# Kernel tuning notes

Measured on AMD Instinct MI355X. Metric: run time of the kernel, lower is better.

The kernel has to match this reference:

```python
import jax, jax.numpy as jnp
import numpy as np

N_NODES = 100000
N_EDGES = 1600000
IN_FEATS = 128
H_FEATS = 128
NUM_CLASSES = 1


def setup_inputs() -> dict:
    key = jax.random.key(0)
    ks = jax.random.split(key, 12)
    node_feat = jax.random.normal(ks[0], (N_NODES, IN_FEATS), dtype=jnp.float32)
    edge_feat = jax.random.normal(ks[1], (N_EDGES, 1), dtype=jnp.float32)
    src = jax.random.randint(ks[2], (N_EDGES,), 0, N_NODES)
    dst = jax.random.randint(ks[3], (N_EDGES,), 0, N_NODES)
    d_in1 = 2 * IN_FEATS + 1
    d_mid = 2 * H_FEATS + 1
    s1 = 1.0 / np.sqrt(d_in1)
    sm = 1.0 / np.sqrt(d_mid)
    W1 = jax.random.uniform(ks[4], (d_in1, H_FEATS), jnp.float32, -s1, s1)
    b1 = jax.random.uniform(ks[5], (H_FEATS,), jnp.float32, -s1, s1)
    Wmid = jax.random.uniform(ks[6], (8, d_mid, H_FEATS), jnp.float32, -sm, sm)
    bmid = jax.random.uniform(ks[7], (8, H_FEATS), jnp.float32, -sm, sm)
    W2 = jax.random.uniform(ks[8], (d_mid, NUM_CLASSES), jnp.float32, -sm, sm)
    b2 = jax.random.uniform(ks[9], (NUM_CLASSES,), jnp.float32, -sm, sm)
    return {"node_feat": node_feat, "edge_feat": edge_feat, "src": src, "dst": dst,
            "W1": W1, "b1": b1, "Wmid": Wmid, "bmid": bmid, "W2": W2, "b2": b2}


def _sage_conv(hn, he, src, dst, W, b):
    # copy_u + sum: aggregate source node features at destination nodes
    hn_aggr = jax.ops.segment_sum(hn[src], dst, num_segments=N_NODES)
    # copy_e + sum: aggregate edge features at destination nodes -> [N, 1]
    he_aggr = jax.ops.segment_sum(he, dst, num_segments=N_NODES)
    h_total = jnp.concatenate([hn, hn_aggr, he_aggr], axis=1)
    return h_total @ W + b


def reference(node_feat, edge_feat, src, dst, W1, b1, Wmid, bmid, W2, b2):
    h = _sage_conv(node_feat, edge_feat, src, dst, W1, b1)
    h = jax.nn.relu(h) + h
    # mid layers 1-4: relu residual
    for i in range(4):
        h = _sage_conv(h, edge_feat, src, dst, Wmid[i], bmid[i])
        h = jax.nn.relu(h) + h
    # mid layer 5: sigmoid (no residual)
    h = _sage_conv(h, edge_feat, src, dst, Wmid[4], bmid[4])
    h = jax.nn.sigmoid(h)
    # mid layers 6-7: relu residual
    for i in range(5, 7):
        h = _sage_conv(h, edge_feat, src, dst, Wmid[i], bmid[i])
        h = jax.nn.relu(h) + h
    # mid layer 8: sigmoid (no residual)
    h = _sage_conv(h, edge_feat, src, dst, Wmid[7], bmid[7])
    h = jax.nn.sigmoid(h)
    # output layer
    h = _sage_conv(h, edge_feat, src, dst, W2, b2)
    return h
```

## Files before the change

kernel.cpp:

```cpp
#include <hip/hip_runtime.h>

#define N_NODES 100000
#define N_EDGES 1600000
#define HF 128
#define BCAP 64

typedef unsigned int uint;
typedef __attribute__((ext_vector_type(8))) short short8;
typedef __attribute__((ext_vector_type(4))) float f32x4;

__device__ __forceinline__ unsigned short f2bf(float f) {
    uint u = __float_as_uint(f);
    uint r = (u + 0x7fff + ((u >> 16) & 1)) >> 16;
    return (unsigned short)r;
}
__device__ __forceinline__ float bf2f_u(uint bits16) {
    return __uint_as_float(bits16 << 16);
}


__global__ void fill_bucket_kernel(const int* __restrict__ src, const int* __restrict__ dst,
                                   const float* __restrict__ ef, int* __restrict__ cur,
                                   int* __restrict__ cs, float* __restrict__ efb, int base) {
    const int Q = N_EDGES / 8;
    int i = blockIdx.x * blockDim.x + threadIdx.x;
    if (i >= Q) return;
    int d[4], s[4]; float f[4];
    #pragma unroll
    for (int k = 0; k < 4; ++k) {
        int e = base + i + k * Q;
        d[k] = dst[e]; s[k] = src[e]; f[k] = ef[e];
    }
    int p[4];
    #pragma unroll
    for (int k = 0; k < 4; ++k) p[k] = atomicAdd(&cur[d[k]], 1);
    #pragma unroll
    for (int k = 0; k < 4; ++k)
        if (p[k] < BCAP) {
            cs[(size_t)d[k] * BCAP + p[k]]  = s[k];
            efb[(size_t)d[k] * BCAP + p[k]] = f[k];
        }
}

__global__ void he_kernel(const float* __restrict__ efb, const int* __restrict__ cnt,
                          float* __restrict__ he) {
    int t = threadIdx.x;
    int node = blockIdx.x * 16 + (t >> 4);
    int gl = t & 15;
    if (node >= N_NODES) return;
    int cn = cnt[node]; if (cn > BCAP) cn = BCAP;
    const float* bk = efb + (size_t)node * BCAP;
    float s = 0.f;
    for (int e = gl; e < cn; e += 16) s += bk[e];
    s += __shfl_xor(s, 1); s += __shfl_xor(s, 2);
    s += __shfl_xor(s, 4); s += __shfl_xor(s, 8);
    if (gl == 0) he[node] = s;
}


__global__ void conv_h_kernel(const float* __restrict__ in, unsigned short* __restrict__ out) {
    int i = (blockIdx.x * 256 + threadIdx.x) * 4;
    float4 v = *(const float4*)(in + i);
    uint2 o;
    o.x = (uint)f2bf(v.x) | ((uint)f2bf(v.y) << 16);
    o.y = (uint)f2bf(v.z) | ((uint)f2bf(v.w) << 16);
    *(uint2*)(out + i) = o;
}

__global__ void conv_w_kernel(const float* __restrict__ W1, const float* __restrict__ Wmid,
                              unsigned short* __restrict__ Wt) {
    int id = blockIdx.x * 256 + threadIdx.x;
    if (id >= 9 * 32768) return;
    int layer = id >> 15;
    int rem = id & 32767;
    int kc = rem >> 10;
    int c  = (rem >> 3) & 127;
    int e  = rem & 7;
    const float* Wl = (layer == 0) ? W1 : Wmid + (size_t)(layer - 1) * 257 * 128;
    Wt[(size_t)layer * 32768 + rem] = f2bf(Wl[(size_t)(kc * 8 + e) * 128 + c]);
}

__global__ void conv_wcb_kernel(const float* __restrict__ W1, const float* __restrict__ b1,
                                const float* __restrict__ Wmid, const float* __restrict__ bmid,
                                float* __restrict__ wcarr, float* __restrict__ barr) {
    int id = blockIdx.x * 256 + threadIdx.x;
    if (id >= 9 * 128) return;
    int layer = id >> 7, c = id & 127;
    const float* Wl = (layer == 0) ? W1 : Wmid + (size_t)(layer - 1) * 257 * 128;
    const float* bl = (layer == 0) ? b1 : bmid + (size_t)(layer - 1) * 128;
    wcarr[id] = Wl[256 * 128 + c];
    barr[id]  = bl[c];
}


__device__ __forceinline__ void accum8(float* lo, float* hi, uint4 v) {
    lo[0] += __uint_as_float(v.x << 16); hi[0] += __uint_as_float(v.x & 0xffff0000u);
    lo[1] += __uint_as_float(v.y << 16); hi[1] += __uint_as_float(v.y & 0xffff0000u);
    lo[2] += __uint_as_float(v.z << 16); hi[2] += __uint_as_float(v.z & 0xffff0000u);
    lo[3] += __uint_as_float(v.w << 16); hi[3] += __uint_as_float(v.w & 0xffff0000u);
}

__launch_bounds__(256, 6)
__global__ void fused_layer_kernel(const unsigned short* __restrict__ X,
                                   unsigned short* __restrict__ Y,
                                   const int* __restrict__ cnt,
                                   const int* __restrict__ cs,
                                   const float* __restrict__ he,
                                   const unsigned short* __restrict__ Wt,
                                   const float* __restrict__ wcarr,
                                   const float* __restrict__ barr,
                                   int mode) {
    __shared__ short gtile[64 * 128];
    int t = threadIdx.x;
    int row0 = blockIdx.x * 64;
    int gl = t & 15;
    const uint4* hu = (const uint4*)X;
    const uint NM1 = N_NODES - 1;

    for (int pass = 0; pass < 4; ++pass) {
        int r = pass * 16 + (t >> 4);
        int node = row0 + r;
        float alo[4] = {0.f,0.f,0.f,0.f}, ahi[4] = {0.f,0.f,0.f,0.f};
        float blo[4] = {0.f,0.f,0.f,0.f}, bhi[4] = {0.f,0.f,0.f,0.f};
        if (node < N_NODES) {
            int cn = cnt[node]; if (cn > BCAP) cn = BCAP;
            const int4* bk4 = (const int4*)(cs + (size_t)node * BCAP);
            int4 q0 = bk4[0], q1 = bk4[1];
            for (int e = 0; e < cn; e += 8) {
                int4 c0 = q0, c1 = q1;
                if (e + 8 < cn) {
                    int b = (e + 8) >> 2;
                    q0 = bk4[b]; q1 = bk4[b + 1];
                }
                uint i0 = min((uint)c0.x, NM1), i1 = min((uint)c0.y, NM1);
                uint i2 = min((uint)c0.z, NM1), i3 = min((uint)c0.w, NM1);
                uint i4 = min((uint)c1.x, NM1), i5 = min((uint)c1.y, NM1);
                uint i6 = min((uint)c1.z, NM1), i7 = min((uint)c1.w, NM1);
                uint4 v0 = hu[(size_t)i0 * 16 + gl];
                uint4 v1 = hu[(size_t)i1 * 16 + gl];
                uint4 v2 = hu[(size_t)i2 * 16 + gl];
                uint4 v3 = hu[(size_t)i3 * 16 + gl];
                uint4 v4 = hu[(size_t)i4 * 16 + gl];
                uint4 v5 = hu[(size_t)i5 * 16 + gl];
                uint4 v6 = hu[(size_t)i6 * 16 + gl];
                uint4 v7 = hu[(size_t)i7 * 16 + gl];
                accum8(alo, ahi, v0);
                if (e + 1 < cn) accum8(blo, bhi, v1);
                if (e + 2 < cn) accum8(alo, ahi, v2);
                if (e + 3 < cn) accum8(blo, bhi, v3);
                if (e + 4 < cn) accum8(alo, ahi, v4);
                if (e + 5 < cn) accum8(blo, bhi, v5);
                if (e + 6 < cn) accum8(alo, ahi, v6);
                if (e + 7 < cn) accum8(blo, bhi, v7);
            }
        }
        uint4 o;
        o.x = (uint)f2bf(alo[0] + blo[0]) | ((uint)f2bf(ahi[0] + bhi[0]) << 16);
        o.y = (uint)f2bf(alo[1] + blo[1]) | ((uint)f2bf(ahi[1] + bhi[1]) << 16);
        o.z = (uint)f2bf(alo[2] + blo[2]) | ((uint)f2bf(ahi[2] + bhi[2]) << 16);
        o.w = (uint)f2bf(alo[3] + blo[3]) | ((uint)f2bf(ahi[3] + bhi[3]) << 16);
        int off = r * 256 + gl * 16;
        off ^= (r & 7) << 4;
        *(uint4*)((char*)gtile + off) = o;
    }
    __syncthreads();

    int w = t >> 6, lane = t & 63;
    int l15 = lane & 15, l4 = lane >> 4;
    int rloc = (w >> 1) * 32;
    int rb = row0 + rloc;
    int cb = (w & 1) * 64;

    f32x4 acc[2][4] = {};

    #pragma unroll
    for (int ks = 0; ks < 8; ++ks) {
        int kk = (ks & 3) * 32 + l4 * 8;
        short8 a[2];
        if (ks < 4) {
            #pragma unroll
            for (int ra = 0; ra < 2; ++ra) {
                int row = rb + ra * 16 + l15;
                if (row > N_NODES - 1) row = N_NODES - 1;
                a[ra] = *(const short8*)((const short*)X + (size_t)row * 128 + kk);
            }
        } else {
            #pragma unroll
            for (int ra = 0; ra < 2; ++ra) {
                int r = rloc + ra * 16 + l15;
                int off = r * 256 + kk * 2;
                off ^= (r & 7) << 4;
                a[ra] = *(const short8*)((const char*)gtile + off);
            }
        }
        short8 b[4];
        const short* wt = (const short*)Wt + (size_t)(ks * 4 + l4) * 1024;
        #pragma unroll
        for (int cf = 0; cf < 4; ++cf) {
            int c = cb + cf * 16 + l15;
            b[cf] = *(const short8*)(wt + c * 8);
        }
        #pragma unroll
        for (int cf = 0; cf < 4; ++cf)
            #pragma unroll
            for (int ra = 0; ra < 2; ++ra)
                acc[ra][cf] = __builtin_amdgcn_mfma_f32_16x16x32_bf16(a[ra], b[cf], acc[ra][cf], 0, 0, 0);
    }

    float wcv[4], bbv[4];
    #pragma unroll
    for (int cf = 0; cf < 4; ++cf) {
        int c = cb + cf * 16 + l15;
        wcv[cf] = wcarr[c];
        bbv[cf] = barr[c];
    }
    #pragma unroll
    for (int ra = 0; ra < 2; ++ra) {
        #pragma unroll
        for (int j = 0; j < 4; ++j) {
            int row = rb + ra * 16 + l4 * 4 + j;
            if (row >= N_NODES) continue;
            float hv = he[row];
            #pragma unroll
            for (int cf = 0; cf < 4; ++cf) {
                int c = cb + cf * 16 + l15;
                float z = acc[ra][cf][j] + hv * wcv[cf] + bbv[cf];
                if (mode == 0) z += fmaxf(z, 0.f);
                else           z = 1.f / (1.f + __expf(-z));
                Y[(size_t)row * 128 + c] = f2bf(z);
            }
        }
    }
}


__global__ void dot_kernel(const unsigned short* __restrict__ h, const float* __restrict__ W2,
                           float* __restrict__ p) {
    int t = threadIdx.x;
    int node = blockIdx.x * 16 + (t >> 4);
    int gl = t & 15;
    if (node >= N_NODES) return;
    uint4 v = ((const uint4*)h)[(size_t)node * 16 + gl];
    const float* wseg = W2 + 128 + gl * 8;
    float s = bf2f_u(v.x & 0xffffu) * wseg[0] + bf2f_u(v.x >> 16) * wseg[1]
            + bf2f_u(v.y & 0xffffu) * wseg[2] + bf2f_u(v.y >> 16) * wseg[3]
            + bf2f_u(v.z & 0xffffu) * wseg[4] + bf2f_u(v.z >> 16) * wseg[5]
            + bf2f_u(v.w & 0xffffu) * wseg[6] + bf2f_u(v.w >> 16) * wseg[7];
    s += __shfl_xor(s, 1); s += __shfl_xor(s, 2);
    s += __shfl_xor(s, 4); s += __shfl_xor(s, 8);
    if (gl == 0) p[node] = s;
}

__global__ void final2_kernel(const unsigned short* __restrict__ h, const float* __restrict__ p,
                              const int* __restrict__ cnt, const int* __restrict__ cs,
                              const float* __restrict__ he, const float* __restrict__ W2,
                              const float* __restrict__ b2, float* __restrict__ out) {
    int t = threadIdx.x;
    int node = blockIdx.x * 16 + (t >> 4);
    int gl = t & 15;
    if (node >= N_NODES) return;
    uint4 v = ((const uint4*)h)[(size_t)node * 16 + gl];
    const float* wseg = W2 + gl * 8;
    float s = bf2f_u(v.x & 0xffffu) * wseg[0] + bf2f_u(v.x >> 16) * wseg[1]
            + bf2f_u(v.y & 0xffffu) * wseg[2] + bf2f_u(v.y >> 16) * wseg[3]
            + bf2f_u(v.z & 0xffffu) * wseg[4] + bf2f_u(v.z >> 16) * wseg[5]
            + bf2f_u(v.w & 0xffffu) * wseg[6] + bf2f_u(v.w >> 16) * wseg[7];
    int cn = cnt[node]; if (cn > BCAP) cn = BCAP;
    const int* bk = cs + (size_t)node * BCAP;
    for (int e = gl; e < cn; e += 16) s += p[bk[e]];
    s += __shfl_xor(s, 1); s += __shfl_xor(s, 2);
    s += __shfl_xor(s, 4); s += __shfl_xor(s, 8);
    if (gl == 0) out[node] = s + he[node] * W2[256] + b2[0];
}


extern "C" void kernel_launch(void* const* d_in, const int* in_sizes, int n_in,
                              void* d_out, int out_size, void* d_ws, size_t ws_size,
                              hipStream_t stream) {
    const float* node_feat = (const float*)d_in[0];
    const float* edge_feat = (const float*)d_in[1];
    const int*   src  = (const int*)d_in[2];
    const int*   dst  = (const int*)d_in[3];
    const float* W1   = (const float*)d_in[4];
    const float* b1   = (const float*)d_in[5];
    const float* Wmid = (const float*)d_in[6];
    const float* bmid = (const float*)d_in[7];
    const float* W2   = (const float*)d_in[8];
    const float* b2   = (const float*)d_in[9];
    float* out = (float*)d_out;

    char* ws = (char*)d_ws;
    size_t off = 0;
    auto carve = [&](size_t bytes) {
        void* p = ws + off;
        off = (off + bytes + 255) & ~(size_t)255;
        return p;
    };
    int*   cur  = (int*)carve((size_t)N_NODES * 4);
    float* he   = (float*)carve((size_t)N_NODES * 4);
    int*   cs   = (int*)carve((size_t)N_NODES * BCAP * 4);
    float* efb  = (float*)carve((size_t)N_NODES * BCAP * 4);
    unsigned short* h0 = (unsigned short*)carve((size_t)N_NODES * HF * 2);
    unsigned short* h1 = (unsigned short*)carve((size_t)N_NODES * HF * 2);
    unsigned short* Wt = (unsigned short*)carve((size_t)9 * 32768 * 2);
    float* wcarr = (float*)carve((size_t)9 * 128 * 4);
    float* barr  = (float*)carve((size_t)9 * 128 * 4);
    float* pbuf  = (float*)carve((size_t)N_NODES * 4);
    (void)ws_size; (void)in_sizes; (void)n_in; (void)out_size;

    hipMemsetAsync(cur, 0, (size_t)N_NODES * 4, stream);
    const int fillGrid = (N_EDGES / 8 + 255) / 256;
    fill_bucket_kernel<<<dim3(fillGrid), dim3(256), 0, stream>>>(
        src, dst, edge_feat, cur, cs, efb, 0);
    fill_bucket_kernel<<<dim3(fillGrid), dim3(256), 0, stream>>>(
        src, dst, edge_feat, cur, cs, efb, N_EDGES / 2);
    he_kernel<<<dim3((N_NODES + 15) / 16), dim3(256), 0, stream>>>(efb, cur, he);

    conv_h_kernel<<<dim3(12500), dim3(256), 0, stream>>>(node_feat, h0);
    conv_w_kernel<<<dim3((9 * 32768 + 255) / 256), dim3(256), 0, stream>>>(W1, Wmid, Wt);
    conv_wcb_kernel<<<dim3(5), dim3(256), 0, stream>>>(W1, b1, Wmid, bmid, wcarr, barr);

    const int gemmGrid = (N_NODES + 63) / 64;
    unsigned short* hbuf[2] = { h0, h1 };

    for (int L = 0; L < 9; ++L) {
        int mode = (L == 5 || L == 8) ? 1 : 0;
        fused_layer_kernel<<<dim3(gemmGrid), dim3(256), 0, stream>>>(
            hbuf[L & 1], hbuf[(L + 1) & 1], cur, cs, he,
            Wt + (size_t)L * 32768, wcarr + L * 128, barr + L * 128, mode);
    }
    const unsigned short* hf = hbuf[1];
    dot_kernel<<<dim3((N_NODES + 15) / 16), dim3(256), 0, stream>>>(hf, W2, pbuf);
    final2_kernel<<<dim3((N_NODES + 15) / 16), dim3(256), 0, stream>>>(
        hf, pbuf, cur, cs, he, W2, b2, out);
}
```

Before: 829.8 us.

## Bucket edges by source-node group and pack source index with bf16 edge feature

Edges for each destination are split into 8 sub-buckets by source-id range, so the gather loop in each layer walks groups in order and all rows of a block touch similar regions of the feature table at the same time, aiming for better L2 locality. Each bucket entry packs the 17-bit source index with a truncated bf16 edge feature into one word, which removes the separate edge-feature bucket array. The cost is a larger bucket array and an 8x larger counter array, plus a per-group cap of 16 that can drop edges whenever a group overflows. Group boundaries are not synchronised across threads, so the intended locality relies on per-group timing lining up on its own.

```diff
diff --git a/kernel.cpp b/kernel.cpp
--- a/kernel.cpp
+++ b/kernel.cpp
@@ -3,7 +3,9 @@
 #define N_NODES 100000
 #define N_EDGES 1600000
 #define HF 128
-#define BCAP 64
+#define NGRP 8
+#define GCAP 16
+#define BKSZ (NGRP * GCAP)
 
 typedef unsigned int uint;
 typedef __attribute__((ext_vector_type(8))) short short8;
@@ -17,41 +19,48 @@
 __device__ __forceinline__ float bf2f_u(uint bits16) {
     return __uint_as_float(bits16 << 16);
 }
+__device__ __forceinline__ uint src_group(uint s) {
+    return (uint)(((unsigned long long)s * 687195ull) >> 33);
+}
 
 
 __global__ void fill_bucket_kernel(const int* __restrict__ src, const int* __restrict__ dst,
-                                   const float* __restrict__ ef, int* __restrict__ cur,
-                                   int* __restrict__ cs, float* __restrict__ efb, int base) {
+                                   const float* __restrict__ ef, int* __restrict__ gcnt,
+                                   uint* __restrict__ cs, int base) {
     const int Q = N_EDGES / 8;
     int i = blockIdx.x * blockDim.x + threadIdx.x;
     if (i >= Q) return;
-    int d[4], s[4]; float f[4];
+    int d[4]; uint ent[4], g[4];
     #pragma unroll
     for (int k = 0; k < 4; ++k) {
         int e = base + i + k * Q;
-        d[k] = dst[e]; s[k] = src[e]; f[k] = ef[e];
+        d[k] = dst[e];
+        uint s = (uint)src[e];
+        ent[k] = (s << 15) | ((uint)f2bf(ef[e]) >> 1);
+        g[k] = src_group(s);
     }
     int p[4];
     #pragma unroll
-    for (int k = 0; k < 4; ++k) p[k] = atomicAdd(&cur[d[k]], 1);
+    for (int k = 0; k < 4; ++k) p[k] = atomicAdd(&gcnt[d[k] * NGRP + g[k]], 1);
     #pragma unroll
     for (int k = 0; k < 4; ++k)
-        if (p[k] < BCAP) {
-            cs[(size_t)d[k] * BCAP + p[k]]  = s[k];
-            efb[(size_t)d[k] * BCAP + p[k]] = f[k];
-        }
-}
-
-__global__ void he_kernel(const float* __restrict__ efb, const int* __restrict__ cnt,
+        if (p[k] < GCAP)
+            cs[(size_t)d[k] * BKSZ + g[k] * GCAP + p[k]] = ent[k];
+}
+
+__global__ void he_kernel(const uint* __restrict__ cs, const int* __restrict__ gcnt,
                           float* __restrict__ he) {
     int t = threadIdx.x;
     int node = blockIdx.x * 16 + (t >> 4);
     int gl = t & 15;
     if (node >= N_NODES) return;
-    int cn = cnt[node]; if (cn > BCAP) cn = BCAP;
-    const float* bk = efb + (size_t)node * BCAP;
+    const uint* bk = cs + (size_t)node * BKSZ;
     float s = 0.f;
-    for (int e = gl; e < cn; e += 16) s += bk[e];
+    #pragma unroll
+    for (int g = 0; g < NGRP; ++g) {
+        int cn = gcnt[node * NGRP + g]; if (cn > GCAP) cn = GCAP;
+        if (gl < cn) s += __uint_as_float((bk[g * GCAP + gl] & 0x7fffu) << 17);
+    }
     s += __shfl_xor(s, 1); s += __shfl_xor(s, 2);
     s += __shfl_xor(s, 4); s += __shfl_xor(s, 8);
     if (gl == 0) he[node] = s;
@@ -93,18 +102,18 @@
 }
 
 
-__device__ __forceinline__ void accum8(float* lo, float* hi, uint4 v) {
-    lo[0] += __uint_as_float(v.x << 16); hi[0] += __uint_as_float(v.x & 0xffff0000u);
-    lo[1] += __uint_as_float(v.y << 16); hi[1] += __uint_as_float(v.y & 0xffff0000u);
-    lo[2] += __uint_as_float(v.z << 16); hi[2] += __uint_as_float(v.z & 0xffff0000u);
-    lo[3] += __uint_as_float(v.w << 16); hi[3] += __uint_as_float(v.w & 0xffff0000u);
+__device__ __forceinline__ void accum8lh(float* a, uint4 v) {
+    a[0] += __uint_as_float(v.x << 16); a[4] += __uint_as_float(v.x & 0xffff0000u);
+    a[1] += __uint_as_float(v.y << 16); a[5] += __uint_as_float(v.y & 0xffff0000u);
+    a[2] += __uint_as_float(v.z << 16); a[6] += __uint_as_float(v.z & 0xffff0000u);
+    a[3] += __uint_as_float(v.w << 16); a[7] += __uint_as_float(v.w & 0xffff0000u);
 }
 
 __launch_bounds__(256, 6)
 __global__ void fused_layer_kernel(const unsigned short* __restrict__ X,
                                    unsigned short* __restrict__ Y,
-                                   const int* __restrict__ cnt,
-                                   const int* __restrict__ cs,
+                                   const int* __restrict__ gcnt,
+                                   const uint* __restrict__ cs,
                                    const float* __restrict__ he,
                                    const unsigned short* __restrict__ Wt,
                                    const float* __restrict__ wcarr,
@@ -117,48 +126,45 @@
     const uint4* hu = (const uint4*)X;
     const uint NM1 = N_NODES - 1;
 
-    for (int pass = 0; pass < 4; ++pass) {
-        int r = pass * 16 + (t >> 4);
-        int node = row0 + r;
-        float alo[4] = {0.f,0.f,0.f,0.f}, ahi[4] = {0.f,0.f,0.f,0.f};
-        float blo[4] = {0.f,0.f,0.f,0.f}, bhi[4] = {0.f,0.f,0.f,0.f};
-        if (node < N_NODES) {
-            int cn = cnt[node]; if (cn > BCAP) cn = BCAP;
-            const int4* bk4 = (const int4*)(cs + (size_t)node * BCAP);
-            int4 q0 = bk4[0], q1 = bk4[1];
-            for (int e = 0; e < cn; e += 8) {
-                int4 c0 = q0, c1 = q1;
-                if (e + 8 < cn) {
-                    int b = (e + 8) >> 2;
-                    q0 = bk4[b]; q1 = bk4[b + 1];
-                }
-                uint i0 = min((uint)c0.x, NM1), i1 = min((uint)c0.y, NM1);
-                uint i2 = min((uint)c0.z, NM1), i3 = min((uint)c0.w, NM1);
-                uint i4 = min((uint)c1.x, NM1), i5 = min((uint)c1.y, NM1);
-                uint i6 = min((uint)c1.z, NM1), i7 = min((uint)c1.w, NM1);
+    float acc[4][8];
+    #pragma unroll
+    for (int p4 = 0; p4 < 4; ++p4)
+        #pragma unroll
+        for (int j = 0; j < 8; ++j) acc[p4][j] = 0.f;
+
+    for (int g = 0; g < NGRP; ++g) {
+        #pragma unroll
+        for (int pass = 0; pass < 4; ++pass) {
+            int node = row0 + pass * 16 + (t >> 4);
+            if (node >= N_NODES) continue;
+            int cn = gcnt[node * NGRP + g]; if (cn > GCAP) cn = GCAP;
+            if (cn == 0) continue;
+            const uint* bk = cs + (size_t)node * BKSZ + g * GCAP;
+            uint4 q = *(const uint4*)bk;
+            for (int e = 0; e < cn; e += 4) {
+                uint4 c = q;
+                if (e + 4 < cn) q = *(const uint4*)(bk + e + 4);
+                uint i0 = min(c.x >> 15, NM1), i1 = min(c.y >> 15, NM1);
+                uint i2 = min(c.z >> 15, NM1), i3 = min(c.w >> 15, NM1);
                 uint4 v0 = hu[(size_t)i0 * 16 + gl];
                 uint4 v1 = hu[(size_t)i1 * 16 + gl];
                 uint4 v2 = hu[(size_t)i2 * 16 + gl];
                 uint4 v3 = hu[(size_t)i3 * 16 + gl];
-                uint4 v4 = hu[(size_t)i4 * 16 + gl];
-                uint4 v5 = hu[(size_t)i5 * 16 + gl];
-                uint4 v6 = hu[(size_t)i6 * 16 + gl];
-                uint4 v7 = hu[(size_t)i7 * 16 + gl];
-                accum8(alo, ahi, v0);
-                if (e + 1 < cn) accum8(blo, bhi, v1);
-                if (e + 2 < cn) accum8(alo, ahi, v2);
-                if (e + 3 < cn) accum8(blo, bhi, v3);
-                if (e + 4 < cn) accum8(alo, ahi, v4);
-                if (e + 5 < cn) accum8(blo, bhi, v5);
-                if (e + 6 < cn) accum8(alo, ahi, v6);
-                if (e + 7 < cn) accum8(blo, bhi, v7);
+                accum8lh(acc[pass], v0);
+                if (e + 1 < cn) accum8lh(acc[pass], v1);
+                if (e + 2 < cn) accum8lh(acc[pass], v2);
+                if (e + 3 < cn) accum8lh(acc[pass], v3);
             }
         }
+    }
+    #pragma unroll
+    for (int pass = 0; pass < 4; ++pass) {
+        int r = pass * 16 + (t >> 4);
         uint4 o;
-        o.x = (uint)f2bf(alo[0] + blo[0]) | ((uint)f2bf(ahi[0] + bhi[0]) << 16);
-        o.y = (uint)f2bf(alo[1] + blo[1]) | ((uint)f2bf(ahi[1] + bhi[1]) << 16);
-        o.z = (uint)f2bf(alo[2] + blo[2]) | ((uint)f2bf(ahi[2] + bhi[2]) << 16);
-        o.w = (uint)f2bf(alo[3] + blo[3]) | ((uint)f2bf(ahi[3] + bhi[3]) << 16);
+        o.x = (uint)f2bf(acc[pass][0]) | ((uint)f2bf(acc[pass][4]) << 16);
+        o.y = (uint)f2bf(acc[pass][1]) | ((uint)f2bf(acc[pass][5]) << 16);
+        o.z = (uint)f2bf(acc[pass][2]) | ((uint)f2bf(acc[pass][6]) << 16);
+        o.w = (uint)f2bf(acc[pass][3]) | ((uint)f2bf(acc[pass][7]) << 16);
         int off = r * 256 + gl * 16;
         off ^= (r & 7) << 4;
         *(uint4*)((char*)gtile + off) = o;
@@ -171,7 +177,7 @@
     int rb = row0 + rloc;
     int cb = (w & 1) * 64;
 
-    f32x4 acc[2][4] = {};
+    f32x4 macc[2][4] = {};
 
     #pragma unroll
     for (int ks = 0; ks < 8; ++ks) {
@@ -204,7 +210,7 @@
         for (int cf = 0; cf < 4; ++cf)
             #pragma unroll
             for (int ra = 0; ra < 2; ++ra)
-                acc[ra][cf] = __builtin_amdgcn_mfma_f32_16x16x32_bf16(a[ra], b[cf], acc[ra][cf], 0, 0, 0);
+                macc[ra][cf] = __builtin_amdgcn_mfma_f32_16x16x32_bf16(a[ra], b[cf], macc[ra][cf], 0, 0, 0);
     }
 
     float wcv[4], bbv[4];
@@ -224,7 +230,7 @@
             #pragma unroll
             for (int cf = 0; cf < 4; ++cf) {
                 int c = cb + cf * 16 + l15;
-                float z = acc[ra][cf][j] + hv * wcv[cf] + bbv[cf];
+                float z = macc[ra][cf][j] + hv * wcv[cf] + bbv[cf];
                 if (mode == 0) z += fmaxf(z, 0.f);
                 else           z = 1.f / (1.f + __expf(-z));
                 Y[(size_t)row * 128 + c] = f2bf(z);
@@ -252,7 +258,7 @@
 }
 
 __global__ void final2_kernel(const unsigned short* __restrict__ h, const float* __restrict__ p,
-                              const int* __restrict__ cnt, const int* __restrict__ cs,
+                              const int* __restrict__ gcnt, const uint* __restrict__ cs,
                               const float* __restrict__ he, const float* __restrict__ W2,
                               const float* __restrict__ b2, float* __restrict__ out) {
     int t = threadIdx.x;
@@ -265,9 +271,13 @@
             + bf2f_u(v.y & 0xffffu) * wseg[2] + bf2f_u(v.y >> 16) * wseg[3]
             + bf2f_u(v.z & 0xffffu) * wseg[4] + bf2f_u(v.z >> 16) * wseg[5]
             + bf2f_u(v.w & 0xffffu) * wseg[6] + bf2f_u(v.w >> 16) * wseg[7];
-    int cn = cnt[node]; if (cn > BCAP) cn = BCAP;
-    const int* bk = cs + (size_t)node * BCAP;
-    for (int e = gl; e < cn; e += 16) s += p[bk[e]];
+    const uint NM1 = N_NODES - 1;
+    const uint* bk = cs + (size_t)node * BKSZ;
+    #pragma unroll
+    for (int g = 0; g < NGRP; ++g) {
+        int cn = gcnt[node * NGRP + g]; if (cn > GCAP) cn = GCAP;
+        if (gl < cn) s += p[min(bk[g * GCAP + gl] >> 15, NM1)];
+    }
     s += __shfl_xor(s, 1); s += __shfl_xor(s, 2);
     s += __shfl_xor(s, 4); s += __shfl_xor(s, 8);
     if (gl == 0) out[node] = s + he[node] * W2[256] + b2[0];
@@ -296,10 +306,9 @@
         off = (off + bytes + 255) & ~(size_t)255;
         return p;
     };
-    int*   cur  = (int*)carve((size_t)N_NODES * 4);
+    int*   gcnt = (int*)carve((size_t)N_NODES * NGRP * 4);
     float* he   = (float*)carve((size_t)N_NODES * 4);
-    int*   cs   = (int*)carve((size_t)N_NODES * BCAP * 4);
-    float* efb  = (float*)carve((size_t)N_NODES * BCAP * 4);
+    uint*  cs   = (uint*)carve((size_t)N_NODES * BKSZ * 4);
     unsigned short* h0 = (unsigned short*)carve((size_t)N_NODES * HF * 2);
     unsigned short* h1 = (unsigned short*)carve((size_t)N_NODES * HF * 2);
     unsigned short* Wt = (unsigned short*)carve((size_t)9 * 32768 * 2);
@@ -308,13 +317,13 @@
     float* pbuf  = (float*)carve((size_t)N_NODES * 4);
     (void)ws_size; (void)in_sizes; (void)n_in; (void)out_size;
 
-    hipMemsetAsync(cur, 0, (size_t)N_NODES * 4, stream);
+    hipMemsetAsync(gcnt, 0, (size_t)N_NODES * NGRP * 4, stream);
     const int fillGrid = (N_EDGES / 8 + 255) / 256;
     fill_bucket_kernel<<<dim3(fillGrid), dim3(256), 0, stream>>>(
-        src, dst, edge_feat, cur, cs, efb, 0);
+        src, dst, edge_feat, gcnt, cs, 0);
     fill_bucket_kernel<<<dim3(fillGrid), dim3(256), 0, stream>>>(
-        src, dst, edge_feat, cur, cs, efb, N_EDGES / 2);
-    he_kernel<<<dim3((N_NODES + 15) / 16), dim3(256), 0, stream>>>(efb, cur, he);
+        src, dst, edge_feat, gcnt, cs, N_EDGES / 2);
+    he_kernel<<<dim3((N_NODES + 15) / 16), dim3(256), 0, stream>>>(cs, gcnt, he);
 
     conv_h_kernel<<<dim3(12500), dim3(256), 0, stream>>>(node_feat, h0);
     conv_w_kernel<<<dim3((9 * 32768 + 255) / 256), dim3(256), 0, stream>>>(W1, Wmid, Wt);
@@ -326,11 +335,11 @@
     for (int L = 0; L < 9; ++L) {
         int mode = (L == 5 || L == 8) ? 1 : 0;
         fused_layer_kernel<<<dim3(gemmGrid), dim3(256), 0, stream>>>(
-            hbuf[L & 1], hbuf[(L + 1) & 1], cur, cs, he,
+            hbuf[L & 1], hbuf[(L + 1) & 1], gcnt, cs, he,
             Wt + (size_t)L * 32768, wcarr + L * 128, barr + L * 128, mode);
     }
     const unsigned short* hf = hbuf[1];
     dot_kernel<<<dim3((N_NODES + 15) / 16), dim3(256), 0, stream>>>(hf, W2, pbuf);
     final2_kernel<<<dim3((N_NODES + 15) / 16), dim3(256), 0, stream>>>(
-        hf, pbuf, cur, cs, he, W2, b2, out);
-}
+        hf, pbuf, gcnt, cs, he, W2, b2, out);
+}
```

Result: slower. 1.276 ms (+53.7%).
